# Kernel tuning notes

Hardware: AMD Instinct MI355X
Metric: run time of the kernel (lower is better)

The kernel has to match this reference:

```python
import jax, jax.numpy as jnp
import numpy as np

# Model dims (match init_kwargs cfg)
B, C_IN, L = 16, 3, 1024
D_MODEL, N_LAYERS = 256, 4
D_STATE, D_CONV, EXPAND = 16, 4, 2
D_INNER = EXPAND * D_MODEL            # 512
DT_RANK = (D_MODEL + 15) // 16        # 16 (mamba_ssm 'auto' rank)


def setup_inputs() -> dict:
    key = jax.random.key(0)
    ks = jax.random.split(key, 10)
    def rn(k, shape, scale):
        return jax.random.normal(k, shape, jnp.float32) * scale
    inp = {
        "x": jax.random.normal(ks[0], (B, C_IN, L), jnp.float32),
        # input stem: Conv1d(3 -> d_model, k=3, pad=1)
        "stem_w": rn(ks[1], (D_MODEL, C_IN, 3), 0.3),
        "stem_b": jnp.zeros((D_MODEL,), jnp.float32),
        # per-layer params, stacked on leading layer dim
        "norm_g": jnp.ones((N_LAYERS, D_MODEL), jnp.float32),
        "norm_b": jnp.zeros((N_LAYERS, D_MODEL), jnp.float32),
        "in_proj_w": rn(ks[2], (N_LAYERS, 2 * D_INNER, D_MODEL), 0.02),
        "conv_w": rn(ks[3], (N_LAYERS, D_INNER, D_CONV), 0.2),
        "conv_b": jnp.zeros((N_LAYERS, D_INNER), jnp.float32),
        "x_proj_w": rn(ks[4], (N_LAYERS, DT_RANK + 2 * D_STATE, D_INNER), 0.02),
        "dt_w": rn(ks[5], (N_LAYERS, D_INNER, DT_RANK), 0.05),
        "dt_b": jnp.full((N_LAYERS, D_INNER), -4.6, jnp.float32),  # softplus ~= 0.01
        "A_log": jnp.log(jnp.broadcast_to(
            jnp.arange(1, D_STATE + 1, dtype=jnp.float32), (N_LAYERS, D_INNER, D_STATE))),
        "Dp": jnp.ones((N_LAYERS, D_INNER), jnp.float32),
        "out_w": rn(ks[6], (N_LAYERS, D_MODEL, D_INNER), 0.02),
        # final norm + output head Conv1d(d_model -> 1, k=1)
        "fnorm_g": jnp.ones((D_MODEL,), jnp.float32),
        "fnorm_b": jnp.zeros((D_MODEL,), jnp.float32),
        "head_w": rn(ks[7], (1, D_MODEL), 0.05),
        "head_b": jnp.zeros((1,), jnp.float32),
    }
    return inp


def _layernorm(x, g, b, eps=1e-5):
    mu = jnp.mean(x, axis=-1, keepdims=True)
    var = jnp.mean((x - mu) ** 2, axis=-1, keepdims=True)
    return (x - mu) * jax.lax.rsqrt(var + eps) * g + b


def _silu(x):
    return x * jax.nn.sigmoid(x)


def _selective_scan(u, delta, A, Bm, Cm, D):
    # u, delta: [B, L, di]; Bm, Cm: [B, L, ds]; A: [di, ds]; D: [di]
    # h_t = exp(delta_t * A) * h_{t-1} + (delta_t * u_t) * B_t ; y_t = <C_t, h_t>
    def step(h, t):
        d_t, B_t, C_t, u_t = t  # [B,di], [B,ds], [B,ds], [B,di]
        h = h * jnp.exp(d_t[..., None] * A) + (d_t * u_t)[..., None] * B_t[:, None, :]
        return h, jnp.einsum('bds,bs->bd', h, C_t)
    h0 = jnp.zeros((u.shape[0], A.shape[0], A.shape[1]), u.dtype)
    xs = (jnp.moveaxis(delta, 1, 0), jnp.moveaxis(Bm, 1, 0),
          jnp.moveaxis(Cm, 1, 0), jnp.moveaxis(u, 1, 0))
    _, ys = jax.lax.scan(step, h0, xs)            # ys: [L, B, di]
    return jnp.moveaxis(ys, 0, 1) + u * D


def _mamba(x, in_w, cw, cb, xw, dtw, dtb, A_log, Dp, ow):
    # x: [B, L, d_model]
    xz = jnp.einsum('bld,ed->ble', x, in_w)       # [B, L, 2*di]
    xin, z = jnp.split(xz, 2, axis=-1)
    # causal depthwise conv over time
    xc = jnp.moveaxis(xin, 1, 2)                  # [B, di, L]
    xc = jax.lax.conv_general_dilated(
        xc, cw[:, None, :], (1,), [(D_CONV - 1, 0)],
        feature_group_count=D_INNER,
        dimension_numbers=('NCH', 'OIH', 'NCH')) + cb[None, :, None]
    xin = _silu(jnp.moveaxis(xc, 1, 2))           # [B, L, di]
    proj = jnp.einsum('bld,ed->ble', xin, xw)     # [B, L, dt_rank + 2*ds]
    dt = proj[..., :DT_RANK]
    Bm = proj[..., DT_RANK:DT_RANK + D_STATE]
    Cm = proj[..., DT_RANK + D_STATE:]
    delta = jax.nn.softplus(jnp.einsum('blr,dr->bld', dt, dtw) + dtb)
    A = -jnp.exp(A_log)
    y = _selective_scan(xin, delta, A, Bm, Cm, Dp)
    y = y * _silu(z)
    return jnp.einsum('bld,od->blo', y, ow)       # [B, L, d_model]


def reference(x, stem_w, stem_b, norm_g, norm_b, in_proj_w, conv_w, conv_b,
              x_proj_w, dt_w, dt_b, A_log, Dp, out_w, fnorm_g, fnorm_b,
              head_w, head_b):
    # stem: Conv1d(k=3, same padding) + ReLU
    h = jax.lax.conv_general_dilated(
        x, stem_w, (1,), [(1, 1)],
        dimension_numbers=('NCH', 'OIH', 'NCH')) + stem_b[None, :, None]
    h = jax.nn.relu(h)
    h = jnp.moveaxis(h, 1, 2)                     # [B, L, d_model]
    for i in range(N_LAYERS):
        h = h + _mamba(_layernorm(h, norm_g[i], norm_b[i]),
                       in_proj_w[i], conv_w[i], conv_b[i], x_proj_w[i],
                       dt_w[i], dt_b[i], A_log[i], Dp[i], out_w[i])
    h = _layernorm(h, fnorm_g, fnorm_b)
    out = jnp.einsum('bld,od->blo', h, head_w) + head_b
    return jax.nn.sigmoid(jnp.moveaxis(out, 1, 2))  # [B, 1, L]
```

## Files before the change

kernel.cpp:

```cpp
#include <hip/hip_runtime.h>
#include <math.h>

#define BSZ 16
#define LQ 1024
#define DM 256
#define DI 512
#define NT (BSZ*LQ)

typedef __attribute__((ext_vector_type(8))) short short8;
typedef __attribute__((ext_vector_type(4))) short short4v;
typedef __attribute__((ext_vector_type(4))) float f32x4;

#define AS1(p) (const __attribute__((address_space(1))) void*)(p)
#define AS3(p) (__attribute__((address_space(3))) void*)(p)
#define GLOAD16(g, l) __builtin_amdgcn_global_load_lds(AS1(g), AS3(l), 16, 0, 0)

__device__ __forceinline__ short f2bf(float f) {
  union { float f; unsigned u; } a; a.f = f;
  unsigned r = (a.u + 0x7FFF + ((a.u >> 16) & 1)) >> 16;
  return (short)r;
}
__device__ __forceinline__ float bf2f(short s) {
  union { unsigned u; float f; } a; a.u = ((unsigned)(unsigned short)s) << 16;
  return a.f;
}

__global__ void stem_kernel(const float* __restrict__ x, const float* __restrict__ w,
                            const float* __restrict__ bias, float* __restrict__ h) {
  int idx = blockIdx.x * 256 + threadIdx.x;
  int d = idx & 255;
  int l = (idx >> 8) & 1023;
  int b = idx >> 18;
  float acc = bias[d];
#pragma unroll
  for (int c = 0; c < 3; c++) {
    const float* xr = x + (size_t)(b * 3 + c) * LQ;
    const float* wr = w + (size_t)(d * 3 + c) * 3;
#pragma unroll
    for (int k = 0; k < 3; k++) {
      int t = l + k - 1;
      if (t >= 0 && t < LQ) acc += xr[t] * wr[k];
    }
  }
  h[idx] = fmaxf(acc, 0.f);
}

#define WB_IN 262144
#define WB_XP 32768
#define WB_OUT 131072
#define WB_L (WB_IN + WB_XP + WB_OUT)

__global__ void convert_w(const float* __restrict__ in_w, const float* __restrict__ xp_w,
                          const float* __restrict__ out_w, short* __restrict__ wb) {
  int layer = blockIdx.y;
  int idx = blockIdx.x * 256 + threadIdx.x;
  short* dst = wb + (size_t)layer * WB_L;
  float v;
  if (idx < WB_IN) {
    v = in_w[(size_t)layer * WB_IN + idx];
  } else if (idx < WB_IN + WB_XP) {
    int k = idx - WB_IN; int row = k >> 9, col = k & 511;
    v = (row < 48) ? xp_w[(size_t)layer * 48 * 512 + row * 512 + col] : 0.f;
  } else {
    int k = idx - WB_IN - WB_XP;
    v = out_w[(size_t)layer * WB_OUT + k];
  }
  dst[idx] = f2bf(v);
}

__global__ void ln_kernel(const float* __restrict__ x, const float* __restrict__ g,
                          const float* __restrict__ bv, short* __restrict__ o) {
  int token = blockIdx.x * 4 + (threadIdx.x >> 6);
  int lane = threadIdx.x & 63;
  f32x4 v = *(const f32x4*)(x + (size_t)token * DM + lane * 4);
  float s = v[0] + v[1] + v[2] + v[3];
  float q = v[0]*v[0] + v[1]*v[1] + v[2]*v[2] + v[3]*v[3];
#pragma unroll
  for (int off = 32; off > 0; off >>= 1) {
    s += __shfl_xor(s, off, 64);
    q += __shfl_xor(q, off, 64);
  }
  float mu = s * (1.f / DM);
  float var = q * (1.f / DM) - mu * mu;
  float rs = rsqrtf(var + 1e-5f);
  f32x4 gg = *(const f32x4*)(g + lane * 4);
  f32x4 bb = *(const f32x4*)(bv + lane * 4);
  short4v ov;
#pragma unroll
  for (int k = 0; k < 4; k++) ov[k] = f2bf((v[k] - mu) * rs * gg[k] + bb[k]);
  *(short4v*)(o + (size_t)token * DM + lane * 4) = ov;
}

__global__ __launch_bounds__(256) void gemm_mfma_s16(
    const short* __restrict__ A, int K,
    const short* __restrict__ W,
    short* __restrict__ C0, int ld0,
    short* __restrict__ C1, int ld1,
    int split, int N) {
  __shared__ short As[2][128 * 32];
  __shared__ short Bs[2][128 * 32];
  int tid = threadIdx.x;
  int wave = tid >> 6, lane = tid & 63;
  int bm = blockIdx.y * 128, bn = blockIdx.x * 128;
  int wm = (wave >> 1) * 64, wn = (wave & 1) * 64;

  f32x4 acc[4][4];
#pragma unroll
  for (int i = 0; i < 4; i++)
#pragma unroll
    for (int j = 0; j < 4; j++) { acc[i][j][0]=0.f; acc[i][j][1]=0.f; acc[i][j][2]=0.f; acc[i][j][3]=0.f; }

  int srow = lane >> 2;
  int scol = (lane & 3) * 8;
  const short* Ag = A + (size_t)(bm + wave * 32 + srow) * K + scol;
  const short* Wg = W + (size_t)(bn + wave * 32 + srow) * K + scol;
  short* As0W = As[0] + wave * 32 * 32;
  short* As1W = As[1] + wave * 32 * 32;
  short* Bs0W = Bs[0] + wave * 32 * 32;
  short* Bs1W = Bs[1] + wave * 32 * 32;

  int fr = lane & 15;
  int kg = (lane >> 4) * 8;

  for (int k0 = 0; k0 < K; k0 += 64) {
    GLOAD16(Ag + k0,                         As0W);
    GLOAD16(Ag + k0 + (size_t)16 * K,        As0W + 16 * 32);
    GLOAD16(Ag + k0 + 32,                    As1W);
    GLOAD16(Ag + k0 + 32 + (size_t)16 * K,   As1W + 16 * 32);
    GLOAD16(Wg + k0,                         Bs0W);
    GLOAD16(Wg + k0 + (size_t)16 * K,        Bs0W + 16 * 32);
    GLOAD16(Wg + k0 + 32,                    Bs1W);
    GLOAD16(Wg + k0 + 32 + (size_t)16 * K,   Bs1W + 16 * 32);
    __syncthreads();

#pragma unroll
    for (int ks = 0; ks < 2; ks++) {
      short8 af[4], bf[4];
#pragma unroll
      for (int i = 0; i < 4; i++) af[i] = *(const short8*)&As[ks][(wm + i * 16 + fr) * 32 + kg];
#pragma unroll
      for (int j = 0; j < 4; j++) bf[j] = *(const short8*)&Bs[ks][(wn + j * 16 + fr) * 32 + kg];
#pragma unroll
      for (int i = 0; i < 4; i++)
#pragma unroll
        for (int j = 0; j < 4; j++)
          acc[i][j] = __builtin_amdgcn_mfma_f32_16x16x32_bf16(af[i], bf[j], acc[i][j], 0, 0, 0);
    }
    __syncthreads();
  }

  int cn = lane & 15, cr = (lane >> 4) * 4;
#pragma unroll
  for (int i = 0; i < 4; i++) {
    int row0 = bm + wm + i * 16 + cr;
#pragma unroll
    for (int j = 0; j < 4; j++) {
      int col = bn + wn + j * 16 + cn;
      if (col < N) {
#pragma unroll
        for (int r = 0; r < 4; r++) {
          short* p = (col < split) ? (C0 + (size_t)(row0 + r) * ld0 + col)
                                   : (C1 + (size_t)(row0 + r) * ld1 + (col - split));
          *p = f2bf(acc[i][j][r]);
        }
      }
    }
  }
}

__global__ __launch_bounds__(256) void gemm2_xproj(
    const short* __restrict__ A,
    const short* __restrict__ W,
    float* __restrict__ proj) {
  __shared__ short As[32 * 64];
  __shared__ short Bs[64 * 64];
  int tid = threadIdx.x;
  int wave = tid >> 6, lane = tid & 63;
  int bm = blockIdx.y * 32;
  int wm = (wave >> 1) * 16, wn = (wave & 1) * 32;

  f32x4 acc[2];
  acc[0] = (f32x4){0.f,0.f,0.f,0.f};
  acc[1] = (f32x4){0.f,0.f,0.f,0.f};

  int arow = tid >> 3, akk = (tid & 7) * 8;
  const short* Ag = A + (size_t)(bm + arow) * 512 + akk;
  int fr = lane & 15, kg = (lane >> 4) * 8;

  for (int k0 = 0; k0 < 512; k0 += 64) {
    GLOAD16(Ag + k0, As + tid * 8);
#pragma unroll
    for (int i = 0; i < 2; i++) {
      int c = tid + i * 256;
      int row = c >> 3, kk = (c & 7) * 8;
      GLOAD16(W + (size_t)row * 512 + k0 + kk, Bs + c * 8);
    }
    __syncthreads();

#pragma unroll
    for (int ks = 0; ks < 2; ks++) {
      short8 af = *(const short8*)&As[(wm + fr) * 64 + ks * 32 + kg];
#pragma unroll
      for (int j = 0; j < 2; j++) {
        short8 bf = *(const short8*)&Bs[(wn + j * 16 + fr) * 64 + ks * 32 + kg];
        acc[j] = __builtin_amdgcn_mfma_f32_16x16x32_bf16(af, bf, acc[j], 0, 0, 0);
      }
    }
    __syncthreads();
  }

  int cn = lane & 15, cr = (lane >> 4) * 4;
  int row0 = bm + wm + cr;
#pragma unroll
  for (int j = 0; j < 2; j++) {
    int col = wn + j * 16 + cn;
    if (col < 48) {
#pragma unroll
      for (int r = 0; r < 4; r++)
        proj[(size_t)(row0 + r) * 48 + col] = acc[j][r];
    }
  }
}

__global__ __launch_bounds__(256) void gemm_mfma64(
    const short* __restrict__ A, int K,
    const short* __restrict__ W,
    float* __restrict__ C, int ldc, int N, int accum) {
  __shared__ short As[64 * 64];
  __shared__ short Bs[64 * 64];
  int tid = threadIdx.x;
  int wave = tid >> 6, lane = tid & 63;
  int bm = blockIdx.y * 64, bn = blockIdx.x * 64;
  int wm = (wave >> 1) * 32, wn = (wave & 1) * 32;

  f32x4 acc[2][2];
#pragma unroll
  for (int i = 0; i < 2; i++)
#pragma unroll
    for (int j = 0; j < 2; j++) { acc[i][j][0]=0.f; acc[i][j][1]=0.f; acc[i][j][2]=0.f; acc[i][j][3]=0.f; }

  const short* Ag = A + (size_t)bm * K;
  const short* Wg = W + (size_t)bn * K;
  int fr = lane & 15;
  int kg = (lane >> 4) * 8;

  for (int k0 = 0; k0 < K; k0 += 64) {
#pragma unroll
    for (int i = 0; i < 2; i++) {
      int c = tid + i * 256;
      int row = c >> 3, kk = (c & 7) * 8;
      GLOAD16(Ag + (size_t)row * K + k0 + kk, As + c * 8);
      GLOAD16(Wg + (size_t)row * K + k0 + kk, Bs + c * 8);
    }
    __syncthreads();

#pragma unroll
    for (int ks = 0; ks < 2; ks++) {
      short8 af[2], bf[2];
#pragma unroll
      for (int i = 0; i < 2; i++) af[i] = *(const short8*)&As[(wm + i * 16 + fr) * 64 + ks * 32 + kg];
#pragma unroll
      for (int j = 0; j < 2; j++) bf[j] = *(const short8*)&Bs[(wn + j * 16 + fr) * 64 + ks * 32 + kg];
#pragma unroll
      for (int i = 0; i < 2; i++)
#pragma unroll
        for (int j = 0; j < 2; j++)
          acc[i][j] = __builtin_amdgcn_mfma_f32_16x16x32_bf16(af[i], bf[j], acc[i][j], 0, 0, 0);
    }
    __syncthreads();
  }

  int cn = lane & 15, cr = (lane >> 4) * 4;
#pragma unroll
  for (int i = 0; i < 2; i++) {
    int row0 = bm + wm + i * 16 + cr;
#pragma unroll
    for (int j = 0; j < 2; j++) {
      int col = bn + wn + j * 16 + cn;
      if (col < N) {
#pragma unroll
        for (int r = 0; r < 4; r++) {
          float v = acc[i][j][r];
          float* p = C + (size_t)(row0 + r) * ldc + col;
          if (accum) v += *p;
          *p = v;
        }
      }
    }
  }
}

__global__ void conv_silu_kernel(const short* __restrict__ xcb, const float* __restrict__ cw,
                                 const float* __restrict__ cb, short* __restrict__ xinb) {
  int idx = blockIdx.x * 256 + threadIdx.x;
  int d8 = (idx & 63) * 8;
  int l = (idx >> 6) & 1023;
  int b = idx >> 16;
  int t = b * 1024 + l;
  short8 xv[4];
#pragma unroll
  for (int k = 0; k < 4; k++) {
    if (l + k - 3 >= 0) xv[k] = *(const short8*)(xcb + (size_t)(t + k - 3) * 512 + d8);
    else xv[k] = (short8)0;
  }
  short8 ov;
#pragma unroll
  for (int e = 0; e < 8; e++) {
    f32x4 wv = *(const f32x4*)(cw + (d8 + e) * 4);
    float acc = cb[d8 + e];
#pragma unroll
    for (int k = 0; k < 4; k++) acc += bf2f(xv[k][e]) * wv[k];
    acc = acc / (1.f + __expf(-acc));
    ov[e] = f2bf(acc);
  }
  *(short8*)(xinb + (size_t)t * 512 + d8) = ov;
}

template <int CTRL>
__device__ __forceinline__ float dpp_add(float x) {
  int yi = __builtin_amdgcn_update_dpp(0, __float_as_int(x), CTRL, 0xF, 0xF, true);
  return x + __int_as_float(yi);
}
__device__ __forceinline__ float sum16(float x) {
  x = dpp_add<0xB1>(x);
  x = dpp_add<0x4E>(x);
  x = dpp_add<0x124>(x);
  x = dpp_add<0x128>(x);
  return x;
}

#define TCH 32
__global__ __launch_bounds__(256) void scan_kernel(
    const short* __restrict__ xinb, const float* __restrict__ proj,
    const short* __restrict__ zc,
    const float* __restrict__ dt_w, const float* __restrict__ dt_b,
    const float* __restrict__ A_log, const float* __restrict__ Dp,
    short* __restrict__ ybf) {
  int b  = blockIdx.x >> 5;
  int d0 = (blockIdx.x & 31) << 4;
  int tid = threadIdx.x;
  int ci = tid >> 4;
  int s  = tid & 15;
  int d = d0 + ci;

  __shared__ float sDt[32 * 20];
  __shared__ float sBT[16 * 36];
  __shared__ float sCT[16 * 36];
  __shared__ float sUT[16 * 36];
  __shared__ float sDU[16 * 36];
  __shared__ float sDel[16 * 36];
  __shared__ float sY[32 * 17];

  float Av = -__expf(A_log[(size_t)d * 16 + s]);
  f32x4 wv4[4];
#pragma unroll
  for (int k = 0; k < 4; k++) wv4[k] = *(const f32x4*)&dt_w[(size_t)d * 16 + k * 4];
  float db = dt_b[d];
  float Ddj = Dp[d0 + s];
  float h = 0.f;

  const float* projb = proj + (size_t)b * LQ * 48;
  const short* xinbb = xinb + (size_t)b * LQ * 512 + d0;
  const short* zcb   = zc   + (size_t)b * LQ * 512 + d0;
  short* ybb         = ybf  + (size_t)b * LQ * 512 + d0;

  int tt = tid >> 4, j = tid & 15;

  int tr[6], rr[6];
#pragma unroll
  for (int k = 0; k < 6; k++) { int idx = tid + k * 256; tr[k] = idx / 48; rr[k] = idx - tr[k] * 48; }

  float uv0, uv1, zv0, zv1;
  {
    float pjv[6];
#pragma unroll
    for (int k = 0; k < 6; k++) pjv[k] = projb[tid + k * 256];
    uv0 = bf2f(xinbb[(size_t)tt * 512 + j]);
    uv1 = bf2f(xinbb[(size_t)(tt + 16) * 512 + j]);
    zv0 = bf2f(zcb[(size_t)tt * 512 + j]);
    zv1 = bf2f(zcb[(size_t)(tt + 16) * 512 + j]);
#pragma unroll
    for (int k = 0; k < 6; k++) {
      int r = rr[k], t = tr[k];
      if (r < 16)      sDt[t * 20 + r] = pjv[k];
      else if (r < 32) sBT[(r - 16) * 36 + t] = pjv[k];
      else             sCT[(r - 32) * 36 + t] = pjv[k];
    }
    sUT[j * 36 + tt] = uv0;
    sUT[j * 36 + tt + 16] = uv1;
  }
  __syncthreads();

  const int NCH = LQ / TCH;
  for (int c = 0; c < NCH; c++) {
    int t0 = c * TCH;

    float pjn[6], un0 = 0.f, un1 = 0.f, zn0 = 0.f, zn1 = 0.f;
    if (c + 1 < NCH) {
      const float* g = projb + (t0 + TCH) * 48;
#pragma unroll
      for (int k = 0; k < 6; k++) pjn[k] = g[tid + k * 256];
      un0 = bf2f(xinbb[(size_t)(t0 + TCH + tt) * 512 + j]);
      un1 = bf2f(xinbb[(size_t)(t0 + TCH + tt + 16) * 512 + j]);
      zn0 = bf2f(zcb[(size_t)(t0 + TCH + tt) * 512 + j]);
      zn1 = bf2f(zcb[(size_t)(t0 + TCH + tt + 16) * 512 + j]);
    }

    {
      f32x4 a0 = *(const f32x4*)&sDt[s * 20 + 0];
      f32x4 a1 = *(const f32x4*)&sDt[s * 20 + 4];
      f32x4 a2 = *(const f32x4*)&sDt[s * 20 + 8];
      f32x4 a3 = *(const f32x4*)&sDt[s * 20 + 12];
      f32x4 b0 = *(const f32x4*)&sDt[(s + 16) * 20 + 0];
      f32x4 b1 = *(const f32x4*)&sDt[(s + 16) * 20 + 4];
      f32x4 b2 = *(const f32x4*)&sDt[(s + 16) * 20 + 8];
      f32x4 b3 = *(const f32x4*)&sDt[(s + 16) * 20 + 12];
      float dt0 = db, dt1 = db;
#pragma unroll
      for (int q = 0; q < 4; q++) {
        dt0 += a0[q] * wv4[0][q] + a1[q] * wv4[1][q] + a2[q] * wv4[2][q] + a3[q] * wv4[3][q];
        dt1 += b0[q] * wv4[0][q] + b1[q] * wv4[1][q] + b2[q] * wv4[2][q] + b3[q] * wv4[3][q];
      }
      float de0 = (dt0 > 15.f) ? dt0 : __logf(1.f + __expf(dt0));
      float de1 = (dt1 > 15.f) ? dt1 : __logf(1.f + __expf(dt1));
      float u0 = sUT[ci * 36 + s];
      float u1 = sUT[ci * 36 + s + 16];
      sDel[ci * 36 + s]      = de0;
      sDel[ci * 36 + s + 16] = de1;
      sDU[ci * 36 + s]       = de0 * u0;
      sDU[ci * 36 + s + 16]  = de1 * u1;
    }
    __syncthreads();

    {
      float ee[TCH], cin[TCH];
      f32x4 ct[8];
      {
        f32x4 dl[8], du8[8], bt[8];
#pragma unroll
        for (int k = 0; k < 8; k++) {
          dl[k]  = *(const f32x4*)&sDel[ci * 36 + k * 4];
          du8[k] = *(const f32x4*)&sDU[ci * 36 + k * 4];
          bt[k]  = *(const f32x4*)&sBT[s * 36 + k * 4];
          ct[k]  = *(const f32x4*)&sCT[s * 36 + k * 4];
        }
#pragma unroll
        for (int t = 0; t < TCH; t++) {
          ee[t] = __expf(dl[t >> 2][t & 3] * Av);
          cin[t] = du8[t >> 2][t & 3] * bt[t >> 2][t & 3];
        }
      }
      float pv0 = 0.f, pv1 = 0.f;
#pragma unroll
      for (int t = 0; t < TCH; t++) {
        h = h * ee[t] + cin[t];
        float p = sum16(h * ct[t >> 2][t & 3]);
        if (t < 16) pv0 = (s == t) ? p : pv0;
        else        pv1 = (s == (t - 16)) ? p : pv1;
      }
      sY[s * 17 + ci] = pv0;
      sY[(s + 16) * 17 + ci] = pv1;
    }
    __syncthreads();

    {
      float p0 = sY[tt * 17 + j];
      float p1 = sY[(tt + 16) * 17 + j];
      float y0 = p0 + uv0 * Ddj;
      float y1 = p1 + uv1 * Ddj;
      float g0 = zv0 / (1.f + __expf(-zv0));
      float g1 = zv1 / (1.f + __expf(-zv1));
      ybb[(size_t)(t0 + tt) * 512 + j] = f2bf(y0 * g0);
      ybb[(size_t)(t0 + tt + 16) * 512 + j] = f2bf(y1 * g1);
    }
    if (c + 1 < NCH) {
#pragma unroll
      for (int k = 0; k < 6; k++) {
        int r = rr[k], t = tr[k];
        if (r < 16)      sDt[t * 20 + r] = pjn[k];
        else if (r < 32) sBT[(r - 16) * 36 + t] = pjn[k];
        else             sCT[(r - 32) * 36 + t] = pjn[k];
      }
      sUT[j * 36 + tt] = un0;
      sUT[j * 36 + tt + 16] = un1;
      uv0 = un0; uv1 = un1; zv0 = zn0; zv1 = zn1;
    }
    __syncthreads();
  }
}

__global__ void head_kernel(const float* __restrict__ h, const float* __restrict__ g,
                            const float* __restrict__ bv, const float* __restrict__ hw,
                            const float* __restrict__ hb, float* __restrict__ out) {
  int token = blockIdx.x;
  int d = threadIdx.x;
  float v = h[(size_t)token * DM + d];
  float s = v, q = v * v;
#pragma unroll
  for (int off = 32; off > 0; off >>= 1) {
    s += __shfl_down(s, off, 64);
    q += __shfl_down(q, off, 64);
  }
  __shared__ float ss[4], qq[4], cc[4];
  int lane = d & 63, wid = d >> 6;
  if (lane == 0) { ss[wid] = s; qq[wid] = q; }
  __syncthreads();
  s = ss[0] + ss[1] + ss[2] + ss[3];
  q = qq[0] + qq[1] + qq[2] + qq[3];
  float mu = s * (1.f / DM);
  float var = q * (1.f / DM) - mu * mu;
  float rs = rsqrtf(var + 1e-5f);
  float xn = (v - mu) * rs * g[d] + bv[d];
  float c = xn * hw[d];
#pragma unroll
  for (int off = 32; off > 0; off >>= 1) c += __shfl_down(c, off, 64);
  if (lane == 0) cc[wid] = c;
  __syncthreads();
  if (threadIdx.x == 0) {
    float t = cc[0] + cc[1] + cc[2] + cc[3] + hb[0];
    out[token] = 1.f / (1.f + __expf(-t));
  }
}

extern "C" void kernel_launch(void* const* d_in, const int* in_sizes, int n_in,
                              void* d_out, int out_size, void* d_ws, size_t ws_size,
                              hipStream_t stream) {
  const float* x        = (const float*)d_in[0];
  const float* stem_w   = (const float*)d_in[1];
  const float* stem_b   = (const float*)d_in[2];
  const float* norm_g   = (const float*)d_in[3];
  const float* norm_b   = (const float*)d_in[4];
  const float* in_proj_w= (const float*)d_in[5];
  const float* conv_w   = (const float*)d_in[6];
  const float* conv_b   = (const float*)d_in[7];
  const float* x_proj_w = (const float*)d_in[8];
  const float* dt_w     = (const float*)d_in[9];
  const float* dt_b     = (const float*)d_in[10];
  const float* A_log    = (const float*)d_in[11];
  const float* Dp       = (const float*)d_in[12];
  const float* out_w    = (const float*)d_in[13];
  const float* fnorm_g  = (const float*)d_in[14];
  const float* fnorm_b  = (const float*)d_in[15];
  const float* head_w   = (const float*)d_in[16];
  const float* head_b   = (const float*)d_in[17];

  char* base = (char*)d_ws;
  float* h    = (float*)(base);
  short* xcb  = (short*)(base + ((size_t)16 << 20));
  short* zcb  = (short*)(base + ((size_t)32 << 20));
  short* xnb  = (short*)(base + ((size_t)48 << 20));
  short* xinb = (short*)(base + ((size_t)56 << 20));
  short* ybf  = (short*)(base + ((size_t)72 << 20));
  float* proj = (float*)(base + ((size_t)88 << 20));
  short* wb   = (short*)(base + ((size_t)91 << 20));

  stem_kernel<<<NT, 256, 0, stream>>>(x, stem_w, stem_b, h);

  dim3 gcw(WB_L / 256, 4);
  convert_w<<<gcw, 256, 0, stream>>>(in_proj_w, x_proj_w, out_w, wb);

  for (int i = 0; i < 4; i++) {
    const short* wbl = wb + (size_t)i * WB_L;

    ln_kernel<<<NT / 4, 256, 0, stream>>>(h, norm_g + i * DM, norm_b + i * DM, xnb);

    dim3 g1(8, NT / 128);
    gemm_mfma_s16<<<g1, 256, 0, stream>>>(xnb, 256, wbl, xcb, 512, zcb, 512, 512, 1024);

    conv_silu_kernel<<<NT * DI / (256 * 8), 256, 0, stream>>>(xcb, conv_w + i * DI * 4,
                                                              conv_b + i * DI, xinb);

    dim3 g2(1, NT / 32);
    gemm2_xproj<<<g2, 256, 0, stream>>>(xinb, wbl + WB_IN, proj);

    scan_kernel<<<512, 256, 0, stream>>>(xinb, proj, zcb,
                                         dt_w + (size_t)i * DI * 16, dt_b + i * DI,
                                         A_log + (size_t)i * DI * 16, Dp + i * DI, ybf);

    dim3 g3(4, NT / 64);
    gemm_mfma64<<<g3, 256, 0, stream>>>(ybf, 512, wbl + WB_IN + WB_XP, h, 256, 256, 1);
  }

  head_kernel<<<NT, 256, 0, stream>>>(h, fnorm_g, fnorm_b, head_w, head_b, (float*)d_out);
}
```

Measured before the change: 791.1 us.

## Fuse depthwise conv+SiLU into x_proj GEMM, lighten scan barrier and head kernel

Computes the causal depthwise conv and SiLU inside the x_proj GEMM's A-tile load, writing xinb and staging the tile in padded LDS, removing a separate kernel launch and a re-read of xinb. Replaces one block-wide barrier in the scan with a wave barrier to cut sync cost, which may be unsafe if LDS data is shared across waves. Rewrites the head kernel to process one token per wave with vectorized loads and xor shuffles, avoiding LDS and block barriers.

```diff
diff --git a/kernel.cpp b/kernel.cpp
--- a/kernel.cpp
+++ b/kernel.cpp
@@ -168,38 +168,62 @@
   }
 }
 
-__global__ __launch_bounds__(256) void gemm2_xproj(
-    const short* __restrict__ A,
-    const short* __restrict__ W,
-    float* __restrict__ proj) {
-  __shared__ short As[32 * 64];
+__global__ __launch_bounds__(256) void gemm2_conv(
+    const short* __restrict__ xcb, const float* __restrict__ cw, const float* __restrict__ cb,
+    const short* __restrict__ W, short* __restrict__ xinb, float* __restrict__ proj) {
+  __shared__ short As[32 * 72];
   __shared__ short Bs[64 * 64];
+  __shared__ float sCW[512 * 4];
+  __shared__ float sCB[512];
   int tid = threadIdx.x;
   int wave = tid >> 6, lane = tid & 63;
   int bm = blockIdx.y * 32;
   int wm = (wave >> 1) * 16, wn = (wave & 1) * 32;
 
+  for (int i = tid; i < 2048; i += 256) sCW[i] = cw[i];
+  for (int i = tid; i < 512; i += 256) sCB[i] = cb[i];
+  __syncthreads();
+
   f32x4 acc[2];
   acc[0] = (f32x4){0.f,0.f,0.f,0.f};
   acc[1] = (f32x4){0.f,0.f,0.f,0.f};
 
-  int arow = tid >> 3, akk = (tid & 7) * 8;
-  const short* Ag = A + (size_t)(bm + arow) * 512 + akk;
   int fr = lane & 15, kg = (lane >> 4) * 8;
+  int r = tid >> 3;
+  int cg = (tid & 7) * 8;
+  int t = bm + r;
+  int l = t & 1023;
 
   for (int k0 = 0; k0 < 512; k0 += 64) {
-    GLOAD16(Ag + k0, As + tid * 8);
 #pragma unroll
     for (int i = 0; i < 2; i++) {
       int c = tid + i * 256;
-      int row = c >> 3, kk = (c & 7) * 8;
-      GLOAD16(W + (size_t)row * 512 + k0 + kk, Bs + c * 8);
-    }
+      GLOAD16(W + (size_t)(c >> 3) * 512 + k0 + (c & 7) * 8, Bs + c * 8);
+    }
+    int ch0 = k0 + cg;
+    short8 xv[4];
+#pragma unroll
+    for (int k = 0; k < 4; k++) {
+      if (l + k - 3 >= 0) xv[k] = *(const short8*)(xcb + (size_t)(t + k - 3) * 512 + ch0);
+      else xv[k] = (short8)0;
+    }
+    short8 ov;
+#pragma unroll
+    for (int e = 0; e < 8; e++) {
+      f32x4 wv = *(const f32x4*)&sCW[(ch0 + e) * 4];
+      float a = sCB[ch0 + e];
+#pragma unroll
+      for (int k = 0; k < 4; k++) a += bf2f(xv[k][e]) * wv[k];
+      a = a / (1.f + __expf(-a));
+      ov[e] = f2bf(a);
+    }
+    *(short8*)&As[r * 72 + cg] = ov;
+    *(short8*)(xinb + (size_t)t * 512 + ch0) = ov;
     __syncthreads();
 
 #pragma unroll
     for (int ks = 0; ks < 2; ks++) {
-      short8 af = *(const short8*)&As[(wm + fr) * 64 + ks * 32 + kg];
+      short8 af = *(const short8*)&As[(wm + fr) * 72 + ks * 32 + kg];
 #pragma unroll
       for (int j = 0; j < 2; j++) {
         short8 bf = *(const short8*)&Bs[(wn + j * 16 + fr) * 64 + ks * 32 + kg];
@@ -216,8 +240,8 @@
     int col = wn + j * 16 + cn;
     if (col < 48) {
 #pragma unroll
-      for (int r = 0; r < 4; r++)
-        proj[(size_t)(row0 + r) * 48 + col] = acc[j][r];
+      for (int rr2 = 0; rr2 < 4; rr2++)
+        proj[(size_t)(row0 + rr2) * 48 + col] = acc[j][rr2];
     }
   }
 }
@@ -288,32 +312,6 @@
       }
     }
   }
-}
-
-__global__ void conv_silu_kernel(const short* __restrict__ xcb, const float* __restrict__ cw,
-                                 const float* __restrict__ cb, short* __restrict__ xinb) {
-  int idx = blockIdx.x * 256 + threadIdx.x;
-  int d8 = (idx & 63) * 8;
-  int l = (idx >> 6) & 1023;
-  int b = idx >> 16;
-  int t = b * 1024 + l;
-  short8 xv[4];
-#pragma unroll
-  for (int k = 0; k < 4; k++) {
-    if (l + k - 3 >= 0) xv[k] = *(const short8*)(xcb + (size_t)(t + k - 3) * 512 + d8);
-    else xv[k] = (short8)0;
-  }
-  short8 ov;
-#pragma unroll
-  for (int e = 0; e < 8; e++) {
-    f32x4 wv = *(const f32x4*)(cw + (d8 + e) * 4);
-    float acc = cb[d8 + e];
-#pragma unroll
-    for (int k = 0; k < 4; k++) acc += bf2f(xv[k][e]) * wv[k];
-    acc = acc / (1.f + __expf(-acc));
-    ov[e] = f2bf(acc);
-  }
-  *(short8*)(xinb + (size_t)t * 512 + d8) = ov;
 }
 
 template <int CTRL>
@@ -430,7 +428,7 @@
       sDU[ci * 36 + s]       = de0 * u0;
       sDU[ci * 36 + s + 16]  = de1 * u1;
     }
-    __syncthreads();
+    __builtin_amdgcn_wave_barrier();
 
     {
       float ee[TCH], cin[TCH];
@@ -492,34 +490,27 @@
 __global__ void head_kernel(const float* __restrict__ h, const float* __restrict__ g,
                             const float* __restrict__ bv, const float* __restrict__ hw,
                             const float* __restrict__ hb, float* __restrict__ out) {
-  int token = blockIdx.x;
-  int d = threadIdx.x;
-  float v = h[(size_t)token * DM + d];
-  float s = v, q = v * v;
+  int token = blockIdx.x * 4 + (threadIdx.x >> 6);
+  int lane = threadIdx.x & 63;
+  f32x4 v = *(const f32x4*)(h + (size_t)token * DM + lane * 4);
+  float s = v[0] + v[1] + v[2] + v[3];
+  float q = v[0]*v[0] + v[1]*v[1] + v[2]*v[2] + v[3]*v[3];
 #pragma unroll
   for (int off = 32; off > 0; off >>= 1) {
-    s += __shfl_down(s, off, 64);
-    q += __shfl_down(q, off, 64);
-  }
-  __shared__ float ss[4], qq[4], cc[4];
-  int lane = d & 63, wid = d >> 6;
-  if (lane == 0) { ss[wid] = s; qq[wid] = q; }
-  __syncthreads();
-  s = ss[0] + ss[1] + ss[2] + ss[3];
-  q = qq[0] + qq[1] + qq[2] + qq[3];
+    s += __shfl_xor(s, off, 64);
+    q += __shfl_xor(q, off, 64);
+  }
   float mu = s * (1.f / DM);
-  float var = q * (1.f / DM) - mu * mu;
-  float rs = rsqrtf(var + 1e-5f);
-  float xn = (v - mu) * rs * g[d] + bv[d];
-  float c = xn * hw[d];
-#pragma unroll
-  for (int off = 32; off > 0; off >>= 1) c += __shfl_down(c, off, 64);
-  if (lane == 0) cc[wid] = c;
-  __syncthreads();
-  if (threadIdx.x == 0) {
-    float t = cc[0] + cc[1] + cc[2] + cc[3] + hb[0];
-    out[token] = 1.f / (1.f + __expf(-t));
-  }
+  float rs = rsqrtf(q * (1.f / DM) - mu * mu + 1e-5f);
+  f32x4 gg = *(const f32x4*)(g + lane * 4);
+  f32x4 bb = *(const f32x4*)(bv + lane * 4);
+  f32x4 ww = *(const f32x4*)(hw + lane * 4);
+  float c = 0.f;
+#pragma unroll
+  for (int k = 0; k < 4; k++) c += ((v[k] - mu) * rs * gg[k] + bb[k]) * ww[k];
+#pragma unroll
+  for (int off = 32; off > 0; off >>= 1) c += __shfl_xor(c, off, 64);
+  if (lane == 0) out[token] = 1.f / (1.f + __expf(-(c + hb[0])));
 }
 
 extern "C" void kernel_launch(void* const* d_in, const int* in_sizes, int n_in,
@@ -567,11 +558,9 @@
     dim3 g1(8, NT / 128);
     gemm_mfma_s16<<<g1, 256, 0, stream>>>(xnb, 256, wbl, xcb, 512, zcb, 512, 512, 1024);
 
-    conv_silu_kernel<<<NT * DI / (256 * 8), 256, 0, stream>>>(xcb, conv_w + i * DI * 4,
-                                                              conv_b + i * DI, xinb);
-
     dim3 g2(1, NT / 32);
-    gemm2_xproj<<<g2, 256, 0, stream>>>(xinb, wbl + WB_IN, proj);
+    gemm2_conv<<<g2, 256, 0, stream>>>(xcb, conv_w + i * DI * 4, conv_b + i * DI,
+                                       wbl + WB_IN, xinb, proj);
 
     scan_kernel<<<512, 256, 0, stream>>>(xinb, proj, zcb,
                                          dt_w + (size_t)i * DI * 16, dt_b + i * DI,
@@ -581,5 +570,5 @@
     gemm_mfma64<<<g3, 256, 0, stream>>>(ybf, 512, wbl + WB_IN + WB_XP, h, 256, 256, 1);
   }
 
-  head_kernel<<<NT, 256, 0, stream>>>(h, fnorm_g, fnorm_b, head_w, head_b, (float*)d_out);
-}
+  head_kernel<<<NT / 4, 256, 0, stream>>>(h, fnorm_g, fnorm_b, head_w, head_b, (float*)d_out);
+}
```

Measured after the change: 722.5 us. -8.7%, faster.
